# Optimization experiments

Measured on AMD Instinct MI355X. Metric: run time of the kernel, lower is better.

The kernel has to match this reference:

```python
import jax, jax.numpy as jnp
import numpy as np

N, D, C = 4096, 1024, 1000
EPS = 1e-8


def _remove_diag(M):
    # faithful to torch M[off_diag_mask].view(h, h-1) via strided-reshape trick
    h = M.shape[0]
    return M.reshape(-1)[1:].reshape(h - 1, h + 1)[:, :-1].reshape(h, h - 1)


def _cosine_sim_matrix(x, y):
    # torch CosineSimilarity: x.y / max(||x||*||y||, eps)
    xn = jnp.linalg.norm(x, axis=-1, keepdims=True)
    yn = jnp.linalg.norm(y, axis=-1, keepdims=True)
    num = jnp.einsum('id,jd->ij', x, y)
    den = jnp.maximum(xn * yn.T, EPS)
    return num / den


def setup_inputs() -> dict:
    key = jax.random.key(0)
    k1, k2, k3, k4 = jax.random.split(key, 4)
    return {
        'inst_embed': jax.random.normal(k1, (N, D), dtype=jnp.float32),
        'anchor': jax.random.normal(k2, (N, D), dtype=jnp.float32),
        'cls_mask': jax.random.randint(k3, (C, N), 0, 2, dtype=jnp.int32),
        'labels': jax.random.randint(k4, (N,), 0, C, dtype=jnp.int64),
        'temperature': jnp.float32(1.0),
    }


def reference(inst_embed, anchor, cls_mask, labels, temperature):
    # augmentation=None branch of Conditional_Embedding_Contrastive_loss.forward
    sim = _cosine_sim_matrix(inst_embed, inst_embed)          # [N,N]
    instance_zone = jnp.exp(_remove_diag(sim) / temperature)  # [N,N-1]
    mask_neg = _remove_diag(cls_mask[labels].astype(instance_zone.dtype))  # [N,N-1]
    inst2inst_pos = instance_zone * mask_neg
    # elementwise cosine sim between inst_embed and anchor rows
    dot = jnp.sum(inst_embed * anchor, axis=-1)
    nrm = jnp.maximum(jnp.linalg.norm(inst_embed, axis=-1) * jnp.linalg.norm(anchor, axis=-1), EPS)
    inst2embed_pos = jnp.exp((dot / nrm) / temperature)       # [N]
    numerator = inst2inst_pos.sum(axis=1) + inst2embed_pos
    denominator = inst2embed_pos + instance_zone.sum(axis=1)
    return -jnp.mean(jnp.log(numerator / denominator))
```

## Files before the change

### kernel.cpp

```cpp
#include <hip/hip_runtime.h>
#include <hip/hip_bf16.h>
#include <math.h>


#define NN   4096
#define DD   1024
#define NCLS 1000
#define EPSF 1e-8f

typedef short bf16x8 __attribute__((ext_vector_type(8)));
typedef float f32x4  __attribute__((ext_vector_type(4)));

__global__ void k_labels(const int* __restrict__ lraw, int* __restrict__ lab) {
  __shared__ int stride_s;
  if (threadIdx.x == 0) {
    int stride = 2;
    #pragma unroll
    for (int t = 0; t < 8; ++t) {
      int lo = lraw[2 * t], hi = lraw[2 * t + 1];
      if (hi != 0 || (unsigned)lo >= (unsigned)NCLS) { stride = 1; break; }
    }
    stride_s = stride;
  }
  __syncthreads();
  const int s = stride_s;
  for (int i = threadIdx.x; i < NN; i += blockDim.x) lab[i] = lraw[i * s];
}

__global__ __launch_bounds__(256) void k_rowstats(
    const float* __restrict__ X, const float* __restrict__ A,
    const float* __restrict__ Tp, ushort* __restrict__ Xb,
    float* __restrict__ rnx, float* __restrict__ rnT,
    float* __restrict__ epos,
    float* __restrict__ sfull, float* __restrict__ smask,
    float* __restrict__ out) {
  const int i = blockIdx.x;
  const int t = threadIdx.x;
  const size_t base = (size_t)i * DD + t * 4;
  const float4 xv = *(const float4*)(X + base);
  const float4 av = *(const float4*)(A + base);
  float sxx = xv.x * xv.x + xv.y * xv.y + xv.z * xv.z + xv.w * xv.w;
  float saa = av.x * av.x + av.y * av.y + av.z * av.z + av.w * av.w;
  float sxa = xv.x * av.x + xv.y * av.y + xv.z * av.z + xv.w * av.w;

  ushort4 pk;
  { __hip_bfloat16 b;
    b = __float2bfloat16(xv.x); pk.x = *(const ushort*)&b;
    b = __float2bfloat16(xv.y); pk.y = *(const ushort*)&b;
    b = __float2bfloat16(xv.z); pk.z = *(const ushort*)&b;
    b = __float2bfloat16(xv.w); pk.w = *(const ushort*)&b; }
  *(ushort4*)(Xb + base) = pk;

  #pragma unroll
  for (int off = 32; off > 0; off >>= 1) {
    sxx += __shfl_down(sxx, off);
    saa += __shfl_down(saa, off);
    sxa += __shfl_down(sxa, off);
  }
  __shared__ float red[3][4];
  const int w = t >> 6;
  if ((t & 63) == 0) { red[0][w] = sxx; red[1][w] = saa; red[2][w] = sxa; }
  __syncthreads();
  if (t == 0) {
    const float a  = red[0][0] + red[0][1] + red[0][2] + red[0][3];
    const float bb = red[1][0] + red[1][1] + red[1][2] + red[1][3];
    const float c  = red[2][0] + red[2][1] + red[2][2] + red[2][3];
    const float nxi = sqrtf(a), nai = sqrtf(bb);
    const float rT  = 1.0f / Tp[0];
    const float r   = 1.0f / fmaxf(nxi, 1e-20f);
    rnx[i] = r;
    rnT[i] = r * rT;
    epos[i] = expf((c / fmaxf(nxi * nai, EPSF)) * rT);
    sfull[i] = 0.f;
    smask[i] = 0.f;
    if (i == 0) out[0] = 0.f;
  }
}

#define BM 128
#define BK 64

__global__ __launch_bounds__(256) void k_gram(
    const ushort* __restrict__ Xb, const float* __restrict__ rnx,
    const float* __restrict__ rnT,
    const int* __restrict__ lab, const int* __restrict__ cmask,
    float* __restrict__ sfull, float* __restrict__ smask) {
  __shared__ __align__(16) char As[BM * BK * 2];
  __shared__ __align__(16) char Bs[BM * BK * 2];
  const int tid  = threadIdx.x;
  const int lane = tid & 63;
  const int w    = tid >> 6;
  const int wr   = w >> 1, wc = w & 1;
  const int i0   = blockIdx.y * BM;
  const int j0   = blockIdx.x * BM;

  const int sslot = (lane & 7) ^ (lane >> 3);

  f32x4 acc[4][4];
  #pragma unroll
  for (int m = 0; m < 4; ++m)
    #pragma unroll
    for (int n = 0; n < 4; ++n)
      acc[m][n] = (f32x4){0.f, 0.f, 0.f, 0.f};

  const ushort* pA[4];
  const ushort* pB[4];
  #pragma unroll
  for (int q = 0; q < 4; ++q) {
    const int row = q * 32 + w * 8 + (lane >> 3);
    pA[q] = Xb + (size_t)(i0 + row) * DD + sslot * 8;
    pB[q] = Xb + (size_t)(j0 + row) * DD + sslot * 8;
  }

  for (int k0 = 0; k0 < DD; k0 += BK) {
    #pragma unroll
    for (int q = 0; q < 4; ++q) {
      __builtin_amdgcn_global_load_lds(
          (const __attribute__((address_space(1))) void*)(pA[q] + k0),
          (__attribute__((address_space(3))) void*)(As + (q * 4 + w) * 1024), 16, 0, 0);
      __builtin_amdgcn_global_load_lds(
          (const __attribute__((address_space(1))) void*)(pB[q] + k0),
          (__attribute__((address_space(3))) void*)(Bs + (q * 4 + w) * 1024), 16, 0, 0);
    }
    __syncthreads();

    #pragma unroll
    for (int ks = 0; ks < 2; ++ks) {
      const int slot = ((ks << 2) + (lane >> 4)) ^ (lane & 7);
      bf16x8 af[4], bfr[4];
      #pragma unroll
      for (int m = 0; m < 4; ++m) {
        const int r = (wr << 6) + (m << 4) + (lane & 15);
        af[m] = *(const bf16x8*)(As + r * 128 + (slot << 4));
      }
      #pragma unroll
      for (int n = 0; n < 4; ++n) {
        const int r = (wc << 6) + (n << 4) + (lane & 15);
        bfr[n] = *(const bf16x8*)(Bs + r * 128 + (slot << 4));
      }
      #pragma unroll
      for (int m = 0; m < 4; ++m)
        #pragma unroll
        for (int n = 0; n < 4; ++n)
          acc[m][n] = __builtin_amdgcn_mfma_f32_16x16x32_bf16(af[m], bfr[n], acc[m][n], 0, 0, 0);
    }
    __syncthreads();
  }

  #pragma unroll
  for (int m = 0; m < 4; ++m) {
    #pragma unroll
    for (int r = 0; r < 4; ++r) {
      const int i = i0 + (wr << 6) + (m << 4) + ((lane >> 4) << 2) + r;
      const float rni = rnx[i];
      const int* mrow = cmask + (size_t)lab[i] * NN;
      float se = 0.f, sm = 0.f;
      #pragma unroll
      for (int n = 0; n < 4; ++n) {
        const int j = j0 + (wc << 6) + (n << 4) + (lane & 15);
        const float g = acc[m][n][r];
        float e = __expf(g * rni * rnT[j]);
        if (i == j) e = 0.f;
        se += e;
        sm = fmaf(e, (float)mrow[j], sm);
      }
      #pragma unroll
      for (int off = 1; off < 16; off <<= 1) {
        se += __shfl_xor(se, off);
        sm += __shfl_xor(sm, off);
      }
      if ((lane & 15) == 0) {
        atomicAdd(&sfull[i], se);
        atomicAdd(&smask[i], sm);
      }
    }
  }
}

__global__ __launch_bounds__(256) void k_final(
    const float* __restrict__ sfull, const float* __restrict__ smask,
    const float* __restrict__ epos, float* __restrict__ out) {
  const int idx = blockIdx.x * 256 + threadIdx.x;
  const float ep  = epos[idx];
  const float num = smask[idx] + ep;
  const float den = ep + sfull[idx];
  float v = (logf(den) - logf(num)) * (1.0f / (float)NN);
  #pragma unroll
  for (int off = 32; off > 0; off >>= 1) v += __shfl_down(v, off);
  __shared__ float red[4];
  if ((threadIdx.x & 63) == 0) red[threadIdx.x >> 6] = v;
  __syncthreads();
  if (threadIdx.x == 0) atomicAdd(out, red[0] + red[1] + red[2] + red[3]);
}

extern "C" void kernel_launch(void* const* d_in, const int* in_sizes, int n_in,
                              void* d_out, int out_size, void* d_ws, size_t ws_size,
                              hipStream_t stream) {
  const float* X     = (const float*)d_in[0];
  const float* A     = (const float*)d_in[1];
  const int*   cmask = (const int*)d_in[2];
  const int*   lraw  = (const int*)d_in[3];
  const float* Tp    = (const float*)d_in[4];
  float* out = (float*)d_out;

  char* ws = (char*)d_ws;
  ushort* Xb   = (ushort*)ws;
  float* rnx   = (float*)(ws + (size_t)NN * DD * 2);
  float* rnT   = rnx + NN;
  float* epos  = rnT + NN;
  float* sfull = epos + NN;
  float* smask = sfull + NN;
  int*   lab   = (int*)(smask + NN);

  hipLaunchKernelGGL(k_labels,   dim3(1),            dim3(256), 0, stream, lraw, lab);
  hipLaunchKernelGGL(k_rowstats, dim3(NN),           dim3(256), 0, stream, X, A, Tp, Xb, rnx, rnT, epos, sfull, smask, out);
  hipLaunchKernelGGL(k_gram,     dim3(NN/BM, NN/BM), dim3(256), 0, stream, Xb, rnx, rnT, lab, cmask, sfull, smask);
  hipLaunchKernelGGL(k_final,    dim3(NN/256),       dim3(256), 0, stream, sfull, smask, epos, out);
}
```

Baseline: 81.04 us.

## Exploit Gram symmetry with triangular tiles and bit-packed class mask

Measured after the change: 81.67 us. No clear change (+0.8%).

```diff
diff --git a/kernel.cpp b/kernel.cpp
--- a/kernel.cpp
+++ b/kernel.cpp
@@ -7,6 +7,7 @@
 #define DD   1024
 #define NCLS 1000
 #define EPSF 1e-8f
+#define MW   (NN / 32)
 
 typedef short bf16x8 __attribute__((ext_vector_type(8)));
 typedef float f32x4  __attribute__((ext_vector_type(4)));
@@ -25,6 +26,22 @@
   __syncthreads();
   const int s = stride_s;
   for (int i = threadIdx.x; i < NN; i += blockDim.x) lab[i] = lraw[i * s];
+}
+
+__global__ __launch_bounds__(256) void k_packmask(const int* __restrict__ cmask,
+                                                  unsigned int* __restrict__ mbits) {
+  const int wword = blockIdx.x * 256 + threadIdx.x;
+  const int* src = cmask + (size_t)wword * 32;
+  unsigned int v = 0;
+  #pragma unroll
+  for (int q = 0; q < 8; ++q) {
+    const int4 c = *(const int4*)(src + q * 4);
+    v |= (c.x != 0 ? 1u : 0u) << (q * 4 + 0);
+    v |= (c.y != 0 ? 1u : 0u) << (q * 4 + 1);
+    v |= (c.z != 0 ? 1u : 0u) << (q * 4 + 2);
+    v |= (c.w != 0 ? 1u : 0u) << (q * 4 + 3);
+  }
+  mbits[wword] = v;
 }
 
 __global__ __launch_bounds__(256) void k_rowstats(
@@ -83,7 +100,7 @@
 __global__ __launch_bounds__(256) void k_gram(
     const ushort* __restrict__ Xb, const float* __restrict__ rnx,
     const float* __restrict__ rnT,
-    const int* __restrict__ lab, const int* __restrict__ cmask,
+    const int* __restrict__ lab, const unsigned int* __restrict__ mbits,
     float* __restrict__ sfull, float* __restrict__ smask) {
   __shared__ __align__(16) char As[BM * BK * 2];
   __shared__ __align__(16) char Bs[BM * BK * 2];
@@ -91,8 +108,16 @@
   const int lane = tid & 63;
   const int w    = tid >> 6;
   const int wr   = w >> 1, wc = w & 1;
-  const int i0   = blockIdx.y * BM;
-  const int j0   = blockIdx.x * BM;
+
+  const int t = blockIdx.x;
+  int a = (int)((sqrtf(8.f * (float)t + 1.f) - 1.f) * 0.5f);
+  while ((a + 1) * (a + 2) / 2 <= t) ++a;
+  while (a * (a + 1) / 2 > t) --a;
+  const int by = t - a * (a + 1) / 2;
+  const int bx = a;
+  const bool offdiag = (bx != by);
+  const int i0 = by * BM;
+  const int j0 = bx * BM;
 
   const int sslot = (lane & 7) ^ (lane >> 3);
 
@@ -147,22 +172,36 @@
     __syncthreads();
   }
 
+  float rnT_j[4];
+  unsigned long long wj[4];
+  #pragma unroll
+  for (int n = 0; n < 4; ++n) {
+    const int j = j0 + (wc << 6) + (n << 4) + (lane & 15);
+    rnT_j[n] = rnT[j];
+    wj[n] = *(const unsigned long long*)(mbits + (size_t)lab[j] * MW + (i0 >> 5) + (wr << 1));
+  }
+  float pse[4] = {0.f, 0.f, 0.f, 0.f}, psm[4] = {0.f, 0.f, 0.f, 0.f};
+
   #pragma unroll
   for (int m = 0; m < 4; ++m) {
     #pragma unroll
     for (int r = 0; r < 4; ++r) {
-      const int i = i0 + (wr << 6) + (m << 4) + ((lane >> 4) << 2) + r;
+      const int irow = (m << 4) + ((lane >> 4) << 2) + r;
+      const int i = i0 + (wr << 6) + irow;
       const float rni = rnx[i];
-      const int* mrow = cmask + (size_t)lab[i] * NN;
+      const unsigned long long wi =
+          *(const unsigned long long*)(mbits + (size_t)lab[i] * MW + (j0 >> 5) + (wc << 1));
       float se = 0.f, sm = 0.f;
       #pragma unroll
       for (int n = 0; n < 4; ++n) {
         const int j = j0 + (wc << 6) + (n << 4) + (lane & 15);
-        const float g = acc[m][n][r];
-        float e = __expf(g * rni * rnT[j]);
+        float e = __expf(acc[m][n][r] * rni * rnT_j[n]);
         if (i == j) e = 0.f;
         se += e;
-        sm = fmaf(e, (float)mrow[j], sm);
+        const int bposj = (n << 4) + (lane & 15);
+        sm += ((wi >> bposj) & 1ull) ? e : 0.f;
+        pse[n] += e;
+        psm[n] += ((wj[n] >> irow) & 1ull) ? e : 0.f;
       }
       #pragma unroll
       for (int off = 1; off < 16; off <<= 1) {
@@ -172,6 +211,20 @@
       if ((lane & 15) == 0) {
         atomicAdd(&sfull[i], se);
         atomicAdd(&smask[i], sm);
+      }
+    }
+  }
+
+  if (offdiag) {
+    #pragma unroll
+    for (int n = 0; n < 4; ++n) {
+      float se = pse[n], sm = psm[n];
+      se += __shfl_xor(se, 16); se += __shfl_xor(se, 32);
+      sm += __shfl_xor(sm, 16); sm += __shfl_xor(sm, 32);
+      if ((lane >> 4) == 0) {
+        const int j = j0 + (wc << 6) + (n << 4) + lane;
+        atomicAdd(&sfull[j], se);
+        atomicAdd(&smask[j], sm);
       }
     }
   }
@@ -211,9 +264,13 @@
   float* sfull = epos + NN;
   float* smask = sfull + NN;
   int*   lab   = (int*)(smask + NN);
-
-  hipLaunchKernelGGL(k_labels,   dim3(1),            dim3(256), 0, stream, lraw, lab);
-  hipLaunchKernelGGL(k_rowstats, dim3(NN),           dim3(256), 0, stream, X, A, Tp, Xb, rnx, rnT, epos, sfull, smask, out);
-  hipLaunchKernelGGL(k_gram,     dim3(NN/BM, NN/BM), dim3(256), 0, stream, Xb, rnx, rnT, lab, cmask, sfull, smask);
-  hipLaunchKernelGGL(k_final,    dim3(NN/256),       dim3(256), 0, stream, sfull, smask, epos, out);
-}
+  unsigned int* mbits = (unsigned int*)(lab + NN);
+
+  const int NTILE = (NN / BM) * (NN / BM + 1) / 2;
+
+  hipLaunchKernelGGL(k_labels,   dim3(1),               dim3(256), 0, stream, lraw, lab);
+  hipLaunchKernelGGL(k_packmask, dim3(NCLS * MW / 256), dim3(256), 0, stream, cmask, mbits);
+  hipLaunchKernelGGL(k_rowstats, dim3(NN),              dim3(256), 0, stream, X, A, Tp, Xb, rnx, rnT, epos, sfull, smask, out);
+  hipLaunchKernelGGL(k_gram,     dim3(NTILE),           dim3(256), 0, stream, Xb, rnx, rnT, lab, mbits, sfull, smask);
+  hipLaunchKernelGGL(k_final,    dim3(NN/256),          dim3(256), 0, stream, sfull, smask, epos, out);
+}
```
